# Optimization experiments

Hardware: AMD Instinct MI355X
Metric: run time of the kernel (lower is better)

## Reference

```python
import jax, jax.numpy as jnp
import numpy as np

DIM = 128
NUM_HEADS = 4
HEAD_DIM = DIM // NUM_HEADS
SCALE = HEAD_DIM ** -0.5
D1, D2 = 6, 2
WH, WW = 8, 8
NW = 64
B_ = 256
N1 = D1 * WH * WW  # 384
N2 = D2 * WH * WW  # 128


def _relative_position_index():
    # mirrors the torch buffer construction exactly
    cd_q = np.arange(D1)
    cd_kv = np.arange(0, D1, (D1 + 1) // D2)  # [0, 3]
    ch = np.arange(WH)
    cw = np.arange(WW)
    coords_q = np.stack(np.meshgrid(cd_q, ch, cw, indexing='ij'))   # (3, D1, Wh, Ww)
    coords_kv = np.stack(np.meshgrid(cd_kv, ch, cw, indexing='ij'))  # (3, D2, Wh, Ww)
    fq = coords_q.reshape(3, -1)   # (3, N1)
    fkv = coords_kv.reshape(3, -1)  # (3, N2)
    rel = fq[:, :, None] - fkv[:, None, :]          # (3, N1, N2)
    rel = np.transpose(rel, (1, 2, 0)).copy()        # (N1, N2, 3)
    rel[:, :, 0] += D1 - 1
    rel[:, :, 1] += WH - 1
    rel[:, :, 2] += WW - 1
    rel[:, :, 0] *= (2 * WH - 1) * (2 * WW - 1)
    rel[:, :, 1] *= 2 * WW - 1
    return rel.sum(-1).astype(np.int32)             # (N1, N2)


def setup_inputs() -> dict:
    key = jax.random.key(0)
    ks = jax.random.split(key, 10)
    table_size = (2 * D1 - 1) * (2 * WH - 1) * (2 * WW - 1)  # 2475
    inp = {
        'q': jax.random.normal(ks[0], (B_, N1, DIM), dtype=jnp.float32),
        'kv': jax.random.normal(ks[1], (B_, N2, DIM), dtype=jnp.float32),
        'mask': jax.random.normal(ks[2], (NW, N1, N2), dtype=jnp.float32),
        'q_w': jax.random.normal(ks[3], (DIM, DIM), dtype=jnp.float32) * 0.02,
        'q_b': jax.random.normal(ks[4], (DIM,), dtype=jnp.float32) * 0.02,
        'kv_w': jax.random.normal(ks[5], (2 * DIM, DIM), dtype=jnp.float32) * 0.02,
        'kv_b': jax.random.normal(ks[6], (2 * DIM,), dtype=jnp.float32) * 0.02,
        'proj_w': jax.random.normal(ks[7], (DIM, DIM), dtype=jnp.float32) * 0.02,
        'proj_b': jax.random.normal(ks[8], (DIM,), dtype=jnp.float32) * 0.02,
        'rpb_table': jax.random.normal(ks[9], (table_size, NUM_HEADS), dtype=jnp.float32) * 0.02,
        'rel_index': jnp.asarray(_relative_position_index()),
    }
    return inp


def reference(q, kv, mask, q_w, q_b, kv_w, kv_b, proj_w, proj_b, rpb_table, rel_index):
    B, n1, C = q.shape
    n2 = kv.shape[1]
    H, hd = NUM_HEADS, HEAD_DIM
    q_copy = q
    # projections (torch Linear: x @ W.T + b)
    qp = (q @ q_w.T + q_b).reshape(B, n1, H, hd).transpose(0, 2, 1, 3)          # (B,H,N1,hd)
    kvp = (kv @ kv_w.T + kv_b).reshape(B, n2, 2, H, hd).transpose(2, 0, 3, 1, 4)  # (2,B,H,N2,hd)
    k, v = kvp[0], kvp[1]
    attn = jnp.einsum('bhqd,bhkd->bhqk', qp * SCALE, k)                          # (B,H,N1,N2)
    # gathered relative position bias
    bias = rpb_table[rel_index.reshape(-1)].reshape(n1, n2, H).transpose(2, 0, 1)  # (H,N1,N2)
    attn = attn + bias[None]
    # shifted-window mask add
    nW = mask.shape[0]
    attn = attn.reshape(B // nW, nW, H, n1, n2) + mask[None, :, None]
    attn = attn.reshape(B, H, n1, n2)
    attn = jax.nn.softmax(attn, axis=-1)
    x = jnp.einsum('bhqk,bhkd->bhqd', attn, v).transpose(0, 2, 1, 3).reshape(B, n1, C)
    x = x @ proj_w.T + proj_b
    return (x + q_copy, attn)
```

## Files before the change

### kernel.cpp

```cpp
#include <hip/hip_runtime.h>


typedef _Float16 f16;
typedef _Float16 f16x4 __attribute__((ext_vector_type(4)));
typedef _Float16 f16x8 __attribute__((ext_vector_type(8)));
typedef float    f32x4 __attribute__((ext_vector_type(4)));

#define MFMA16(a, b, c) __builtin_amdgcn_mfma_f32_16x16x32_f16((a), (b), (c), 0, 0, 0)

constexpr int B_  = 256;
constexpr int N1  = 384;
constexpr int N2  = 128;
constexpr int DIM = 128;
constexpr int H_  = 4;
constexpr int HD  = 32;
constexpr float SCALE = 0.17677669529663687f;

__device__ alignas(16) f16  g_qp[(long)B_ * N1 * DIM];
__device__ alignas(16) f16  g_k [(long)B_ * N2 * DIM];
__device__ alignas(16) f16  g_v [(long)B_ * N2 * DIM];
__device__ alignas(16) f16  g_x [(long)B_ * N1 * DIM];
__device__ float g_bias[H_ * N1 * N2];
__device__ alignas(16) f16  g_wq [DIM * DIM];
__device__ alignas(16) f16  g_wkv[2 * DIM * DIM];
__device__ alignas(16) f16  g_wp [DIM * DIM];

__global__ __launch_bounds__(256) void k_wcvt(const float* __restrict__ qw,
                                              const float* __restrict__ kvw,
                                              const float* __restrict__ pw) {
  int i4 = (blockIdx.x * 256 + threadIdx.x) * 4;
  const float* src;
  f16* dst;
  int off;
  if (i4 < 16384)      { src = qw;  dst = g_wq;  off = i4; }
  else if (i4 < 49152) { src = kvw; dst = g_wkv; off = i4 - 16384; }
  else                 { src = pw;  dst = g_wp;  off = i4 - 49152; }
  float4 v = *reinterpret_cast<const float4*>(src + off);
  f16x4 h = {(f16)v.x, (f16)v.y, (f16)v.z, (f16)v.w};
  *reinterpret_cast<f16x4*>(dst + off) = h;
}

__global__ __launch_bounds__(256) void k_bias(const float* __restrict__ tbl,
                                              const int* __restrict__ rel) {
  int g = blockIdx.x * 256 + threadIdx.x;
  int h = g / (N1 * N2);
  int rem = g - h * (N1 * N2);
  g_bias[g] = tbl[rel[rem] * H_ + h];
}


__global__ __launch_bounds__(256, 4) void k_qproj(const float* __restrict__ qin,
                                                  const float* __restrict__ qb) {
  __shared__ alignas(16) f16 As[64 * 136];
  const int tid = threadIdx.x, wv = tid >> 6, l = tid & 63, lr = l & 15, lg = l >> 4;
  const long row0 = (long)blockIdx.x * 64;
  for (int idx = tid; idx < 2048; idx += 256) {
    int r = idx >> 5, c4 = (idx & 31) << 2;
    float4 v = *reinterpret_cast<const float4*>(qin + (row0 + r) * DIM + c4);
    f16x4 h = {(f16)v.x, (f16)v.y, (f16)v.z, (f16)v.w};
    *reinterpret_cast<f16x4*>(&As[r * 136 + c4]) = h;
  }
  __syncthreads();
  f32x4 acc[8] = {};
#pragma unroll
  for (int ks = 0; ks < 4; ++ks) {
    f16x8 a = *reinterpret_cast<const f16x8*>(&As[(wv * 16 + lr) * 136 + ks * 32 + lg * 8]);
#pragma unroll
    for (int j = 0; j < 8; ++j) {
      f16x8 w = *reinterpret_cast<const f16x8*>(&g_wq[(j * 16 + lr) * DIM + ks * 32 + lg * 8]);
      acc[j] = MFMA16(a, w, acc[j]);
    }
  }
  const long rbase = row0 + wv * 16 + lg * 4;
#pragma unroll
  for (int j = 0; j < 8; ++j) {
    int c = j * 16 + lr;
    float bv = qb[c];
#pragma unroll
    for (int r = 0; r < 4; ++r)
      g_qp[(rbase + r) * DIM + c] = (f16)((acc[j][r] + bv) * SCALE);
  }
}

__global__ __launch_bounds__(256, 4) void k_kvproj(const float* __restrict__ kvin,
                                                   const float* __restrict__ kvb) {
  __shared__ alignas(16) f16 As[64 * 136];
  const int tid = threadIdx.x, wv = tid >> 6, l = tid & 63, lr = l & 15, lg = l >> 4;
  const int rb = blockIdx.x & 511, ch = blockIdx.x >> 9;
  const long row0 = (long)rb * 64;
  for (int idx = tid; idx < 2048; idx += 256) {
    int r = idx >> 5, c4 = (idx & 31) << 2;
    float4 v = *reinterpret_cast<const float4*>(kvin + (row0 + r) * DIM + c4);
    f16x4 h = {(f16)v.x, (f16)v.y, (f16)v.z, (f16)v.w};
    *reinterpret_cast<f16x4*>(&As[r * 136 + c4]) = h;
  }
  __syncthreads();
  const f16* W = g_wkv + (long)ch * DIM * DIM;
  f32x4 acc[8] = {};
#pragma unroll
  for (int ks = 0; ks < 4; ++ks) {
    f16x8 a = *reinterpret_cast<const f16x8*>(&As[(wv * 16 + lr) * 136 + ks * 32 + lg * 8]);
#pragma unroll
    for (int j = 0; j < 8; ++j) {
      f16x8 w = *reinterpret_cast<const f16x8*>(&W[(j * 16 + lr) * DIM + ks * 32 + lg * 8]);
      acc[j] = MFMA16(a, w, acc[j]);
    }
  }
  f16* dst = ch ? g_v : g_k;
  const long rbase = row0 + wv * 16 + lg * 4;
#pragma unroll
  for (int j = 0; j < 8; ++j) {
    int c = j * 16 + lr;
    float bv = kvb[ch * DIM + c];
#pragma unroll
    for (int r = 0; r < 4; ++r)
      dst[(rbase + r) * DIM + c] = (f16)(acc[j][r] + bv);
  }
}

__global__ __launch_bounds__(256, 4) void k_attn(const float* __restrict__ mask,
                                                 float* __restrict__ outAttn) {
  __shared__ alignas(16) f16 vT[32 * 136];
  __shared__ alignas(16) f16 pS[64 * 136];
  const int tid = threadIdx.x, wv = tid >> 6, l = tid & 63, lr = l & 15, lg = l >> 4;
  const int h = blockIdx.x >> 8, b = blockIdx.x & 255, wm = b & 63;

  const f16* gk = g_k + (long)b * N2 * DIM + h * HD;
  const f16* gv = g_v + (long)b * N2 * DIM + h * HD;
  const f16* gq = g_qp + (long)b * N1 * DIM + h * HD;
  float* oA = outAttn + ((long)(b * H_ + h)) * N1 * N2;
  const float* mk = mask + (long)wm * N1 * N2;
  const float* bi = g_bias + (long)h * N1 * N2;

  for (int idx = tid; idx < 512; idx += 256) {
    int n2 = idx >> 2, c8 = (idx & 3) * 8;
    f16x8 v = *reinterpret_cast<const f16x8*>(gv + n2 * DIM + c8);
#pragma unroll
    for (int t = 0; t < 8; ++t) vT[(c8 + t) * 136 + n2] = v[t];
  }
  __syncthreads();

  for (int t6 = 0; t6 < 6; ++t6) {
    const int q0 = t6 * 64;
    f16x8 afr = *reinterpret_cast<const f16x8*>(gq + (q0 + wv * 16 + lr) * DIM + lg * 8);
    const f32x4 fz = {};
    f32x4 s[8];
#pragma unroll
    for (int j = 0; j < 8; ++j) {
      f16x8 kf = *reinterpret_cast<const f16x8*>(gk + (j * 16 + lr) * DIM + lg * 8);
      s[j] = MFMA16(afr, kf, fz);
    }
    const int qrb = q0 + wv * 16 + lg * 4;
#pragma unroll
    for (int r = 0; r < 4; ++r) {
      const long off = (long)(qrb + r) * N2 + lr;
#pragma unroll
      for (int j = 0; j < 8; ++j) s[j][r] += bi[off + 16 * j] + mk[off + 16 * j];
      float m = s[0][r];
#pragma unroll
      for (int j = 1; j < 8; ++j) m = fmaxf(m, s[j][r]);
#pragma unroll
      for (int o = 8; o; o >>= 1) m = fmaxf(m, __shfl_xor(m, o));
      float sum = 0.f;
#pragma unroll
      for (int j = 0; j < 8; ++j) { s[j][r] = __expf(s[j][r] - m); sum += s[j][r]; }
#pragma unroll
      for (int o = 8; o; o >>= 1) sum += __shfl_xor(sum, o);
      const float inv = 1.0f / sum;
#pragma unroll
      for (int j = 0; j < 8; ++j) {
        float p = s[j][r] * inv;
        oA[off + 16 * j] = p;
        pS[(wv * 16 + lg * 4 + r) * 136 + 16 * j + lr] = (f16)p;
      }
    }
    f32x4 x0 = {}, x1 = {};
#pragma unroll
    for (int ks = 0; ks < 4; ++ks) {
      f16x8 pa = *reinterpret_cast<const f16x8*>(&pS[(wv * 16 + lr) * 136 + ks * 32 + lg * 8]);
      f16x8 b0 = *reinterpret_cast<const f16x8*>(&vT[lr * 136 + ks * 32 + lg * 8]);
      f16x8 b1 = *reinterpret_cast<const f16x8*>(&vT[(16 + lr) * 136 + ks * 32 + lg * 8]);
      x0 = MFMA16(pa, b0, x0);
      x1 = MFMA16(pa, b1, x1);
    }
    f16* gx = g_x + ((long)b * N1 + q0 + wv * 16 + lg * 4) * DIM + h * HD;
#pragma unroll
    for (int r = 0; r < 4; ++r) {
      gx[r * DIM + lr] = (f16)x0[r];
      gx[r * DIM + 16 + lr] = (f16)x1[r];
    }
  }
}

__global__ __launch_bounds__(256, 4) void k_proj(const float* __restrict__ qin,
                                                 const float* __restrict__ pb,
                                                 float* __restrict__ outX) {
  __shared__ alignas(16) f16 As[64 * 136];
  const int tid = threadIdx.x, wv = tid >> 6, l = tid & 63, lr = l & 15, lg = l >> 4;
  const long row0 = (long)blockIdx.x * 64;
  for (int idx = tid; idx < 1024; idx += 256) {
    int r = idx >> 4, c8 = (idx & 15) * 8;
    *reinterpret_cast<f16x8*>(&As[r * 136 + c8]) =
        *reinterpret_cast<const f16x8*>(g_x + (row0 + r) * DIM + c8);
  }
  __syncthreads();
  f32x4 acc[8] = {};
#pragma unroll
  for (int ks = 0; ks < 4; ++ks) {
    f16x8 a = *reinterpret_cast<const f16x8*>(&As[(wv * 16 + lr) * 136 + ks * 32 + lg * 8]);
#pragma unroll
    for (int j = 0; j < 8; ++j) {
      f16x8 w = *reinterpret_cast<const f16x8*>(&g_wp[(j * 16 + lr) * DIM + ks * 32 + lg * 8]);
      acc[j] = MFMA16(a, w, acc[j]);
    }
  }
  const long rbase = row0 + wv * 16 + lg * 4;
#pragma unroll
  for (int j = 0; j < 8; ++j) {
    int c = j * 16 + lr;
    float bv = pb[c];
#pragma unroll
    for (int r = 0; r < 4; ++r) {
      long idx = (rbase + r) * DIM + c;
      outX[idx] = acc[j][r] + bv + qin[idx];
    }
  }
}

extern "C" void kernel_launch(void* const* d_in, const int* in_sizes, int n_in,
                              void* d_out, int out_size, void* d_ws, size_t ws_size,
                              hipStream_t stream) {
  (void)in_sizes; (void)n_in; (void)out_size; (void)d_ws; (void)ws_size;
  const float* q    = (const float*)d_in[0];
  const float* kv   = (const float*)d_in[1];
  const float* mask = (const float*)d_in[2];
  const float* qw   = (const float*)d_in[3];
  const float* qb   = (const float*)d_in[4];
  const float* kvw  = (const float*)d_in[5];
  const float* kvb  = (const float*)d_in[6];
  const float* pw   = (const float*)d_in[7];
  const float* pb   = (const float*)d_in[8];
  const float* tbl  = (const float*)d_in[9];
  const int*   rel  = (const int*)d_in[10];

  float* outX = (float*)d_out;
  float* outA = outX + (long)B_ * N1 * DIM;

  hipLaunchKernelGGL(k_wcvt,   dim3(64),   dim3(256), 0, stream, qw, kvw, pw);
  hipLaunchKernelGGL(k_bias,   dim3(768),  dim3(256), 0, stream, tbl, rel);
  hipLaunchKernelGGL(k_qproj,  dim3(1536), dim3(256), 0, stream, q, qb);
  hipLaunchKernelGGL(k_kvproj, dim3(1024), dim3(256), 0, stream, kv, kvb);
  hipLaunchKernelGGL(k_attn,   dim3(1024), dim3(256), 0, stream, mask, outA);
  hipLaunchKernelGGL(k_proj,   dim3(1536), dim3(256), 0, stream, q, pb, outX);
}
```

Measured before the change: 483.9 us.

## Fuse attention with output projection and precombine bias+mask in fp16

Attention and the output projection are merged into one kernel: each block handles one batch element and a 64-row query tile, loops over all heads, keeps the per-head output in shared memory, then applies the projection and residual directly. This drops the g_x round trip and one launch. A prep kernel now builds a combined fp16 bias+mask tensor for all heads and windows, halving the per-element bias/mask read inside attention. The cost is that the prep pass itself reads the full mask, writes a large fp16 tensor, and runs lower occupancy (launch bounds 3) with extra syncs per head.

```diff
diff --git a/kernel.cpp b/kernel.cpp
--- a/kernel.cpp
+++ b/kernel.cpp
@@ -2,6 +2,7 @@
 
 
 typedef _Float16 f16;
+typedef _Float16 f16x2 __attribute__((ext_vector_type(2)));
 typedef _Float16 f16x4 __attribute__((ext_vector_type(4)));
 typedef _Float16 f16x8 __attribute__((ext_vector_type(8)));
 typedef float    f32x4 __attribute__((ext_vector_type(4)));
@@ -14,38 +15,45 @@
 constexpr int DIM = 128;
 constexpr int H_  = 4;
 constexpr int HD  = 32;
+constexpr int NW  = 64;
 constexpr float SCALE = 0.17677669529663687f;
 
-__device__ alignas(16) f16  g_qp[(long)B_ * N1 * DIM];
-__device__ alignas(16) f16  g_k [(long)B_ * N2 * DIM];
-__device__ alignas(16) f16  g_v [(long)B_ * N2 * DIM];
-__device__ alignas(16) f16  g_x [(long)B_ * N1 * DIM];
-__device__ float g_bias[H_ * N1 * N2];
-__device__ alignas(16) f16  g_wq [DIM * DIM];
-__device__ alignas(16) f16  g_wkv[2 * DIM * DIM];
-__device__ alignas(16) f16  g_wp [DIM * DIM];
-
-__global__ __launch_bounds__(256) void k_wcvt(const float* __restrict__ qw,
+__device__ alignas(16) f16 g_qp[(long)B_ * N1 * DIM];
+__device__ alignas(16) f16 g_k [(long)B_ * N2 * DIM];
+__device__ alignas(16) f16 g_v [(long)B_ * N2 * DIM];
+__device__ alignas(4)  f16 g_bm[(long)H_ * NW * N1 * N2];
+__device__ alignas(16) f16 g_wq [DIM * DIM];
+__device__ alignas(16) f16 g_wkv[2 * DIM * DIM];
+__device__ alignas(16) f16 g_wp [DIM * DIM];
+
+__global__ __launch_bounds__(256) void k_prep(const float* __restrict__ mask,
+                                              const float* __restrict__ tbl,
+                                              const int* __restrict__ rel,
+                                              const float* __restrict__ qw,
                                               const float* __restrict__ kvw,
                                               const float* __restrict__ pw) {
-  int i4 = (blockIdx.x * 256 + threadIdx.x) * 4;
-  const float* src;
-  f16* dst;
-  int off;
-  if (i4 < 16384)      { src = qw;  dst = g_wq;  off = i4; }
-  else if (i4 < 49152) { src = kvw; dst = g_wkv; off = i4 - 16384; }
-  else                 { src = pw;  dst = g_wp;  off = i4 - 49152; }
-  float4 v = *reinterpret_cast<const float4*>(src + off);
-  f16x4 h = {(f16)v.x, (f16)v.y, (f16)v.z, (f16)v.w};
-  *reinterpret_cast<f16x4*>(dst + off) = h;
-}
-
-__global__ __launch_bounds__(256) void k_bias(const float* __restrict__ tbl,
-                                              const int* __restrict__ rel) {
-  int g = blockIdx.x * 256 + threadIdx.x;
-  int h = g / (N1 * N2);
-  int rem = g - h * (N1 * N2);
-  g_bias[g] = tbl[rel[rem] * H_ + h];
+  if (blockIdx.x < 24576) {
+    long p2 = ((long)blockIdx.x * 256 + threadIdx.x) * 2;
+    int h = (int)(p2 / (NW * N1 * N2));
+    long rem = p2 - (long)h * (NW * N1 * N2);
+    int wm = (int)(rem / (N1 * N2));
+    long qk = rem - (long)wm * (N1 * N2);
+    float2 mk = *reinterpret_cast<const float2*>(mask + (long)wm * N1 * N2 + qk);
+    int r0 = rel[qk], r1 = rel[qk + 1];
+    f16x2 o = {(f16)(tbl[r0 * H_ + h] + mk.x), (f16)(tbl[r1 * H_ + h] + mk.y)};
+    *reinterpret_cast<f16x2*>(g_bm + p2) = o;
+  } else {
+    int i4 = ((blockIdx.x - 24576) * 256 + threadIdx.x) * 4;
+    const float* src;
+    f16* dst;
+    int off;
+    if (i4 < 16384)      { src = qw;  dst = g_wq;  off = i4; }
+    else if (i4 < 49152) { src = kvw; dst = g_wkv; off = i4 - 16384; }
+    else                 { src = pw;  dst = g_wp;  off = i4 - 49152; }
+    float4 v = *reinterpret_cast<const float4*>(src + off);
+    f16x4 h4 = {(f16)v.x, (f16)v.y, (f16)v.z, (f16)v.w};
+    *reinterpret_cast<f16x4*>(dst + off) = h4;
+  }
 }
 
 
@@ -118,44 +126,51 @@
   }
 }
 
-__global__ __launch_bounds__(256, 4) void k_attn(const float* __restrict__ mask,
-                                                 float* __restrict__ outAttn) {
+__global__ __launch_bounds__(256, 3) void k_fused(const float* __restrict__ qin,
+                                                  const float* __restrict__ pb,
+                                                  float* __restrict__ outX,
+                                                  float* __restrict__ outAttn) {
   __shared__ alignas(16) f16 vT[32 * 136];
   __shared__ alignas(16) f16 pS[64 * 136];
+  __shared__ alignas(16) f16 xS[64 * 136];
   const int tid = threadIdx.x, wv = tid >> 6, l = tid & 63, lr = l & 15, lg = l >> 4;
-  const int h = blockIdx.x >> 8, b = blockIdx.x & 255, wm = b & 63;
-
-  const f16* gk = g_k + (long)b * N2 * DIM + h * HD;
-  const f16* gv = g_v + (long)b * N2 * DIM + h * HD;
-  const f16* gq = g_qp + (long)b * N1 * DIM + h * HD;
-  float* oA = outAttn + ((long)(b * H_ + h)) * N1 * N2;
-  const float* mk = mask + (long)wm * N1 * N2;
-  const float* bi = g_bias + (long)h * N1 * N2;
-
-  for (int idx = tid; idx < 512; idx += 256) {
-    int n2 = idx >> 2, c8 = (idx & 3) * 8;
-    f16x8 v = *reinterpret_cast<const f16x8*>(gv + n2 * DIM + c8);
-#pragma unroll
-    for (int t = 0; t < 8; ++t) vT[(c8 + t) * 136 + n2] = v[t];
-  }
-  __syncthreads();
-
-  for (int t6 = 0; t6 < 6; ++t6) {
-    const int q0 = t6 * 64;
-    f16x8 afr = *reinterpret_cast<const f16x8*>(gq + (q0 + wv * 16 + lr) * DIM + lg * 8);
-    const f32x4 fz = {};
+  const int xcd = blockIdx.x & 7, j5 = blockIdx.x >> 3;
+  const int b = xcd + 8 * (j5 / 6), t6 = j5 % 6;
+  const int wm = b & 63, q0 = t6 * 64;
+
+  const f16* gq = g_qp + ((long)b * N1 + q0) * DIM;
+  const f16* gk = g_k + (long)b * N2 * DIM;
+  const f16* gv = g_v + (long)b * N2 * DIM;
+  float* oA = outAttn + (long)b * H_ * N1 * N2;
+  const f32x4 fz = {};
+
+#pragma unroll 1
+  for (int h = 0; h < H_; ++h) {
+    __syncthreads();
+    for (int idx = tid; idx < 512; idx += 256) {
+      int n2 = idx >> 2, c8 = (idx & 3) * 8;
+      f16x8 v = *reinterpret_cast<const f16x8*>(gv + n2 * DIM + h * HD + c8);
+#pragma unroll
+      for (int t = 0; t < 8; ++t) vT[(c8 + t) * 136 + n2] = v[t];
+    }
+    __syncthreads();
+
+    f16x8 afr = *reinterpret_cast<const f16x8*>(gq + (wv * 16 + lr) * DIM + h * HD + lg * 8);
     f32x4 s[8];
 #pragma unroll
     for (int j = 0; j < 8; ++j) {
-      f16x8 kf = *reinterpret_cast<const f16x8*>(gk + (j * 16 + lr) * DIM + lg * 8);
+      f16x8 kf = *reinterpret_cast<const f16x8*>(gk + (j * 16 + lr) * DIM + h * HD + lg * 8);
       s[j] = MFMA16(afr, kf, fz);
     }
-    const int qrb = q0 + wv * 16 + lg * 4;
+
+    const f16* bm = g_bm + ((long)(h * NW + wm) * N1 + q0) * N2;
+    float* oAh = oA + (long)h * N1 * N2;
 #pragma unroll
     for (int r = 0; r < 4; ++r) {
-      const long off = (long)(qrb + r) * N2 + lr;
-#pragma unroll
-      for (int j = 0; j < 8; ++j) s[j][r] += bi[off + 16 * j] + mk[off + 16 * j];
+      const int row = wv * 16 + lg * 4 + r;
+      const f16* bmr = bm + (long)row * N2 + lr;
+#pragma unroll
+      for (int j = 0; j < 8; ++j) s[j][r] += (float)bmr[16 * j];
       float m = s[0][r];
 #pragma unroll
       for (int j = 1; j < 8; ++j) m = fmaxf(m, s[j][r]);
@@ -167,14 +182,16 @@
 #pragma unroll
       for (int o = 8; o; o >>= 1) sum += __shfl_xor(sum, o);
       const float inv = 1.0f / sum;
+      float* oAr = oAh + (long)(q0 + row) * N2 + lr;
 #pragma unroll
       for (int j = 0; j < 8; ++j) {
         float p = s[j][r] * inv;
-        oA[off + 16 * j] = p;
-        pS[(wv * 16 + lg * 4 + r) * 136 + 16 * j + lr] = (f16)p;
+        oAr[16 * j] = p;
+        pS[row * 136 + 16 * j + lr] = (f16)p;
       }
     }
-    f32x4 x0 = {}, x1 = {};
+
+    f32x4 x0 = fz, x1 = fz;
 #pragma unroll
     for (int ks = 0; ks < 4; ++ks) {
       f16x8 pa = *reinterpret_cast<const f16x8*>(&pS[(wv * 16 + lr) * 136 + ks * 32 + lg * 8]);
@@ -183,38 +200,25 @@
       x0 = MFMA16(pa, b0, x0);
       x1 = MFMA16(pa, b1, x1);
     }
-    f16* gx = g_x + ((long)b * N1 + q0 + wv * 16 + lg * 4) * DIM + h * HD;
 #pragma unroll
     for (int r = 0; r < 4; ++r) {
-      gx[r * DIM + lr] = (f16)x0[r];
-      gx[r * DIM + 16 + lr] = (f16)x1[r];
-    }
-  }
-}
-
-__global__ __launch_bounds__(256, 4) void k_proj(const float* __restrict__ qin,
-                                                 const float* __restrict__ pb,
-                                                 float* __restrict__ outX) {
-  __shared__ alignas(16) f16 As[64 * 136];
-  const int tid = threadIdx.x, wv = tid >> 6, l = tid & 63, lr = l & 15, lg = l >> 4;
-  const long row0 = (long)blockIdx.x * 64;
-  for (int idx = tid; idx < 1024; idx += 256) {
-    int r = idx >> 4, c8 = (idx & 15) * 8;
-    *reinterpret_cast<f16x8*>(&As[r * 136 + c8]) =
-        *reinterpret_cast<const f16x8*>(g_x + (row0 + r) * DIM + c8);
-  }
-  __syncthreads();
+      const int row = wv * 16 + lg * 4 + r;
+      xS[row * 136 + h * HD + lr] = (f16)x0[r];
+      xS[row * 136 + h * HD + 16 + lr] = (f16)x1[r];
+    }
+  }
+
   f32x4 acc[8] = {};
 #pragma unroll
   for (int ks = 0; ks < 4; ++ks) {
-    f16x8 a = *reinterpret_cast<const f16x8*>(&As[(wv * 16 + lr) * 136 + ks * 32 + lg * 8]);
+    f16x8 a = *reinterpret_cast<const f16x8*>(&xS[(wv * 16 + lr) * 136 + ks * 32 + lg * 8]);
 #pragma unroll
     for (int j = 0; j < 8; ++j) {
       f16x8 w = *reinterpret_cast<const f16x8*>(&g_wp[(j * 16 + lr) * DIM + ks * 32 + lg * 8]);
       acc[j] = MFMA16(a, w, acc[j]);
     }
   }
-  const long rbase = row0 + wv * 16 + lg * 4;
+  const long rbase = (long)b * N1 + q0 + wv * 16 + lg * 4;
 #pragma unroll
   for (int j = 0; j < 8; ++j) {
     int c = j * 16 + lr;
@@ -246,10 +250,8 @@
   float* outX = (float*)d_out;
   float* outA = outX + (long)B_ * N1 * DIM;
 
-  hipLaunchKernelGGL(k_wcvt,   dim3(64),   dim3(256), 0, stream, qw, kvw, pw);
-  hipLaunchKernelGGL(k_bias,   dim3(768),  dim3(256), 0, stream, tbl, rel);
-  hipLaunchKernelGGL(k_qproj,  dim3(1536), dim3(256), 0, stream, q, qb);
-  hipLaunchKernelGGL(k_kvproj, dim3(1024), dim3(256), 0, stream, kv, kvb);
-  hipLaunchKernelGGL(k_attn,   dim3(1024), dim3(256), 0, stream, mask, outA);
-  hipLaunchKernelGGL(k_proj,   dim3(1536), dim3(256), 0, stream, q, pb, outX);
-}
+  hipLaunchKernelGGL(k_prep,   dim3(24640), dim3(256), 0, stream, mask, tbl, rel, qw, kvw, pw);
+  hipLaunchKernelGGL(k_qproj,  dim3(1536),  dim3(256), 0, stream, q, qb);
+  hipLaunchKernelGGL(k_kvproj, dim3(1024),  dim3(256), 0, stream, kv, kvb);
+  hipLaunchKernelGGL(k_fused,  dim3(1536),  dim3(256), 0, stream, q, pb, outX, outA);
+}
```

New measurement: 452.9 us. -6.4%, faster.
